# Performance work log

Measured on AMD Instinct MI355X. Metric: run time of the kernel, lower is better.

Reference implementation:

```python
import jax, jax.numpy as jnp
import numpy as np

B, S, D_MODEL, H = 4, 1024, 1024, 16
DEPTH = D_MODEL // H


def head_scales():
    # np.arange(0.1, 10 + 0.01, 9.9 / (H - 1)) -> exactly H values from 0.1 to 10.0
    return jnp.asarray(np.arange(0.1, 10 + 0.01, 9.9 / (H - 1)), dtype=jnp.float32)


def setup_inputs() -> dict:
    key = jax.random.key(0)
    ks = jax.random.split(key, 14)
    sd = 1.0 / np.sqrt(D_MODEL)
    inp = {
        "v": jax.random.normal(ks[0], (B, S, D_MODEL), jnp.float32),
        "k": jax.random.normal(ks[1], (B, S, D_MODEL), jnp.float32),
        "q": jax.random.normal(ks[2], (B, S, D_MODEL), jnp.float32),
        # pairwise distance-like weights in [0, 1)
        "weight": jax.random.uniform(ks[3], (B, S, S), jnp.float32),
        # binary padding mask, broadcastable to (B, H, S, S); 1 = masked
        "mask": (jax.random.uniform(ks[4], (B, 1, 1, S)) < 0.1).astype(jnp.float32),
        "Wq": jax.random.normal(ks[5], (D_MODEL, D_MODEL), jnp.float32) * sd,
        "bq": jnp.zeros((D_MODEL,), jnp.float32),
        "Wk": jax.random.normal(ks[6], (D_MODEL, D_MODEL), jnp.float32) * sd,
        "bk": jnp.zeros((D_MODEL,), jnp.float32),
        "Wv": jax.random.normal(ks[7], (D_MODEL, D_MODEL), jnp.float32) * sd,
        "bv": jnp.zeros((D_MODEL,), jnp.float32),
        "Wo": jax.random.normal(ks[8], (D_MODEL, D_MODEL), jnp.float32) * sd,
        "bo": jnp.zeros((D_MODEL,), jnp.float32),
    }
    return inp


def reference(v, k, q, weight, mask, Wq, bq, Wk, bk, Wv, bv, Wo, bo):
    def split_heads(x):  # (B, S, D) -> (B, H, S, depth)
        return x.reshape(B, -1, H, DEPTH).transpose(0, 2, 1, 3)

    qh = split_heads(q @ Wq + bq)
    kh = split_heads(k @ Wk + bk)
    vh = split_heads(v @ Wv + bv)

    # shift_distance[b,h,i,j] = weight[b,i,j] * scale[h]
    scales = head_scales()  # (H,)
    bias = weight[:, None, :, :] * scales[None, :, None, None]  # (B, H, S, S)

    logits = jnp.einsum("bhqd,bhkd->bhqk", qh, kh) / jnp.sqrt(
        jnp.asarray(DEPTH, jnp.float32)
    )
    logits = logits + bias + mask * (-1e9)
    attn = jax.nn.softmax(logits, axis=-1)  # (B, H, S, S)
    out = jnp.einsum("bhqk,bhkd->bhqd", attn, vh)  # (B, H, S, depth)
    out = out.transpose(0, 2, 1, 3).reshape(B, -1, D_MODEL)
    return out @ Wo + bo
```

## Files before the change

kernel.cpp:

```cpp
#include <hip/hip_runtime.h>
#include <hip/hip_fp16.h>

#define DEV __device__ __forceinline__

typedef _Float16 f16x8 __attribute__((ext_vector_type(8)));
typedef _Float16 f16x4 __attribute__((ext_vector_type(4)));
typedef float f32x4 __attribute__((ext_vector_type(4)));

DEV void gload16(void* lds, const void* g) {
  __builtin_amdgcn_global_load_lds((__attribute__((address_space(1))) const void*)g,
                                   (__attribute__((address_space(3))) void*)lds,
                                   16, 0, 0);
}

DEV f32x4 mfma16(f16x8 a, f16x8 b, f32x4 c) {
  return __builtin_amdgcn_mfma_f32_16x16x32_f16(a, b, c, 0, 0, 0);
}

DEV f16x8 cvt8(float4 a, float4 b) {
  f16x8 o;
  o[0] = (_Float16)a.x; o[1] = (_Float16)a.y; o[2] = (_Float16)a.z; o[3] = (_Float16)a.w;
  o[4] = (_Float16)b.x; o[5] = (_Float16)b.y; o[6] = (_Float16)b.z; o[7] = (_Float16)b.w;
  return o;
}

__global__ __launch_bounds__(256) void transw_kernel(
    const float* __restrict__ W0, const float* __restrict__ W1,
    const float* __restrict__ W2, const float* __restrict__ W3,
    _Float16* __restrict__ Wt) {
  __shared__ float tile[32][33];
  const float* W = (blockIdx.z == 0) ? W0 : (blockIdx.z == 1) ? W1
                 : (blockIdx.z == 2) ? W2 : W3;
  _Float16* dst = Wt + (size_t)blockIdx.z * (1024 * 1024);
  const int tx = threadIdx.x & 31, ty = threadIdx.x >> 5;
  const int n0 = blockIdx.x * 32, k0 = blockIdx.y * 32;
#pragma unroll
  for (int i = 0; i < 4; ++i)
    tile[ty + i * 8][tx] = W[(size_t)(k0 + ty + i * 8) * 1024 + n0 + tx];
  __syncthreads();
#pragma unroll
  for (int i = 0; i < 4; ++i)
    dst[(size_t)(n0 + ty + i * 8) * 1024 + k0 + tx] = (_Float16)tile[tx][ty + i * 8];
}

__global__ __launch_bounds__(256) void wcast_kernel(const float* __restrict__ W,
                                                    _Float16* __restrict__ Wh) {
  const size_t i = (size_t)(blockIdx.x * 256 + threadIdx.x) * 8;
  float4 a = *(const float4*)(W + i);
  float4 b = *(const float4*)(W + i + 4);
  *(f16x8*)(Wh + i) = cvt8(a, b);
}

__global__ __launch_bounds__(256) void qkvcast_kernel(
    const float* __restrict__ q, const float* __restrict__ k,
    const float* __restrict__ v, _Float16* __restrict__ Ah) {
  const float* src = (blockIdx.y == 0) ? q : (blockIdx.y == 1) ? k : v;
  _Float16* dst = Ah + (size_t)blockIdx.y * (4096ull * 1024);
  const size_t i = (size_t)(blockIdx.x * 256 + threadIdx.x) * 8;
  float4 a = *(const float4*)(src + i);
  float4 b = *(const float4*)(src + i + 4);
  *(f16x8*)(dst + i) = cvt8(a, b);
}

template <int BM, bool AF32>
DEV void gemm_core(const void* __restrict__ Aptr, const _Float16* __restrict__ Bt,
                   _Float16* Al, _Float16* Bl, int m0, int n0,
                   f32x4 (&acc)[4][4]) {
  constexpr int AS = AF32 ? 40 : 32;
  constexpr int WR = BM / 64, WC = 4 / WR, NI = (128 / WC) / 16;
  const int t = threadIdx.x;
  const int l = t & 63, w = t >> 6;
  const int wr = w / WC, wc = w % WC;
  const int lo = l & 15, lg = l >> 4;

  for (int ks = 0; ks < 1024; ks += 32) {
    __syncthreads();
    gload16(&Bl[t * 8], Bt + (size_t)(n0 + (t >> 2)) * 1024 + ks + (t & 3) * 8);
    gload16(&Bl[(t + 256) * 8], Bt + (size_t)(n0 + (t >> 2) + 64) * 1024 + ks + (t & 3) * 8);
    if constexpr (AF32) {
      const float* Ag = (const float*)Aptr;
      const int row = t >> 1, c0 = (t & 1) * 16;
      const float4* src = (const float4*)(Ag + (size_t)(m0 + row) * 1024 + ks + c0);
      float4 f0 = src[0], f1 = src[1], f2 = src[2], f3 = src[3];
      *(f16x8*)&Al[row * AS + c0] = cvt8(f0, f1);
      *(f16x8*)&Al[row * AS + c0 + 8] = cvt8(f2, f3);
    } else {
      const _Float16* Ag = (const _Float16*)Aptr;
      gload16(&Al[t * 8], Ag + (size_t)(m0 + (t >> 2)) * 1024 + ks + (t & 3) * 8);
      if constexpr (BM == 128)
        gload16(&Al[(t + 256) * 8], Ag + (size_t)(m0 + (t >> 2) + 64) * 1024 + ks + (t & 3) * 8);
    }
    __syncthreads();

    f16x8 af[4], bf[NI];
#pragma unroll
    for (int mi = 0; mi < 4; ++mi)
      af[mi] = *(const f16x8*)&Al[(wr * 64 + mi * 16 + lo) * AS + lg * 8];
#pragma unroll
    for (int ni = 0; ni < NI; ++ni)
      bf[ni] = *(const f16x8*)&Bl[(wc * (NI * 16) + ni * 16 + lo) * 32 + lg * 8];
#pragma unroll
    for (int mi = 0; mi < 4; ++mi)
#pragma unroll
      for (int ni = 0; ni < NI; ++ni)
        acc[mi][ni] = mfma16(af[mi], bf[ni], acc[mi][ni]);
  }
}

template <bool AHALF>
__global__ __launch_bounds__(256) void proj_kernel(
    const _Float16* __restrict__ Ah, const float* __restrict__ qin,
    const float* __restrict__ kin, const float* __restrict__ vin,
    const _Float16* __restrict__ Wt, const float* __restrict__ bq,
    const float* __restrict__ bk, const float* __restrict__ bv,
    _Float16* __restrict__ Qh, _Float16* __restrict__ Kt,
    _Float16* __restrict__ Vt) {
  __shared__ __attribute__((aligned(16))) _Float16 Al[128 * 40];
  __shared__ __attribute__((aligned(16))) _Float16 Bl[128 * 32];
  const int lin = blockIdx.x + (blockIdx.y << 3) + (blockIdx.z << 8);
  const int work = (lin & 7) * 96 + (lin >> 3);
  const int z = work >> 8;
  const int m0 = ((work & 255) >> 3) * 128;
  const int n0 = (work & 7) * 128;

  const _Float16* Bt = Wt + (size_t)z * (1 << 20);
  const float* bias = (z == 0) ? bq : (z == 1) ? bk : bv;
  _Float16* C = (z == 0) ? Qh : (z == 1) ? Kt : Vt;

  f32x4 acc[4][4];
#pragma unroll
  for (int i = 0; i < 4; ++i)
#pragma unroll
    for (int j = 0; j < 4; ++j) acc[i][j] = (f32x4){0.f, 0.f, 0.f, 0.f};
  if constexpr (AHALF) {
    gemm_core<128, false>(Ah + (size_t)z * (4096ull * 1024), Bt, Al, Bl, m0, n0, acc);
  } else {
    const float* A = (z == 0) ? qin : (z == 1) ? kin : vin;
    gemm_core<128, true>(A, Bt, Al, Bl, m0, n0, acc);
  }

  const int l = threadIdx.x & 63, w = threadIdx.x >> 6;
  const int wr = w >> 1, wc = w & 1;
  const int lo = l & 15, lg = l >> 4;
#pragma unroll
  for (int mi = 0; mi < 4; ++mi) {
#pragma unroll
    for (int ni = 0; ni < 4; ++ni) {
      const int col = n0 + wc * 64 + ni * 16 + lo;
      const int rowb = m0 + wr * 64 + mi * 16 + lg * 4;
      const float bc = bias[col];
      const int h = col >> 6, d = col & 63;
#pragma unroll
      for (int r = 0; r < 4; ++r) {
        const float vv = acc[mi][ni][r] + bc;
        const int m = rowb + r;
        const int b = m >> 10, s = m & 1023;
        const size_t slab = (size_t)(b * 16 + h) * 65536;
        if (z == 0) {
          C[slab + (size_t)s * 64 + d] = (_Float16)vv;
        } else if (z == 1) {
          C[slab + (size_t)(s >> 6) * 4096 + (size_t)(s & 63) * 64 +
            (((d >> 3) ^ (s & 7)) << 3) + (d & 7)] = (_Float16)vv;
        } else {
          C[slab + (size_t)(s >> 6) * 4096 + (size_t)d * 64 +
            ((((s >> 3) & 7) ^ (d & 7)) << 3) + (s & 7)] = (_Float16)vv;
        }
      }
    }
  }
}

__global__ __launch_bounds__(256) void outproj_kernel(
    const _Float16* __restrict__ AO, const _Float16* __restrict__ Bt,
    const float* __restrict__ bias, float* __restrict__ out) {
  __shared__ __attribute__((aligned(16))) _Float16 Al[64 * 32];
  __shared__ __attribute__((aligned(16))) _Float16 Bl[128 * 32];
  const int lin = blockIdx.x + (blockIdx.y << 3);
  const int work = (lin & 7) * 64 + (lin >> 3);
  const int m0 = (work >> 3) * 64;
  const int n0 = (work & 7) * 128;
  f32x4 acc[4][4];
#pragma unroll
  for (int i = 0; i < 4; ++i)
#pragma unroll
    for (int j = 0; j < 4; ++j) acc[i][j] = (f32x4){0.f, 0.f, 0.f, 0.f};
  gemm_core<64, false>(AO, Bt, Al, Bl, m0, n0, acc);

  const int l = threadIdx.x & 63, w = threadIdx.x >> 6;
  const int wc = w;
  const int lo = l & 15, lg = l >> 4;
#pragma unroll
  for (int mi = 0; mi < 4; ++mi) {
#pragma unroll
    for (int ni = 0; ni < 2; ++ni) {
      const int col = n0 + wc * 32 + ni * 16 + lo;
      const int rowb = m0 + mi * 16 + lg * 4;
      const float bc = bias[col];
#pragma unroll
      for (int r = 0; r < 4; ++r)
        out[(size_t)(rowb + r) * 1024 + col] = acc[mi][ni][r] + bc;
    }
  }
}

template <int NSPLIT>
__global__ __launch_bounds__(512, 4) void attn_kernel(
    const _Float16* __restrict__ Qh, const _Float16* __restrict__ Kt,
    const _Float16* __restrict__ Vt, const _Float16* __restrict__ Wh,
    const float* __restrict__ mask, void* __restrict__ Oout,
    float2* __restrict__ Sst) {
  __shared__ __attribute__((aligned(16))) _Float16 Kl[2][4096];
  __shared__ __attribute__((aligned(16))) _Float16 Vl[2][4096];
  __shared__ __attribute__((aligned(16))) _Float16 Pl[8][16][72];
  const int t = threadIdx.x, l = t & 63, w = t >> 6;
  const int lo = l & 15, lg = l >> 4;
  const int bh = blockIdx.y, b = bh >> 4, h = bh & 15;
  const int q0w = blockIdx.x * 128 + w * 16;
  const int sp = (NSPLIT > 1) ? blockIdx.z : 0;
  constexpr int NKT = 16 / NSPLIT;
  const int kt0 = sp * NKT;
  constexpr float L2E = 1.44269504089f;
  const float scale = 0.1f + (float)h * (9.9f / 15.0f);
  const float cS = 0.125f * L2E;
  const float cW = scale * L2E;
  const float cM = -1e9f * L2E;
  const _Float16* Kslab = Kt + (size_t)bh * 65536;
  const _Float16* Vslab = Vt + (size_t)bh * 65536;
  const _Float16* Wb = Wh + ((size_t)b << 20);
  const float* Mb = mask + (size_t)b * 1024;
  const int qrow = q0w + lg * 4;
  const int sl = lg ^ (lo & 7);

  const f16x8 qf0 = *(const f16x8*)(Qh + (size_t)bh * 65536 + (q0w + lo) * 64 + lg * 8);
  const f16x8 qf1 = *(const f16x8*)(Qh + (size_t)bh * 65536 + (q0w + lo) * 64 + 32 + lg * 8);

  f32x4 oacc[4];
#pragma unroll
  for (int di = 0; di < 4; ++di) oacc[di] = (f32x4){0.f, 0.f, 0.f, 0.f};
  float mrun[4], lsum[4];
#pragma unroll
  for (int r = 0; r < 4; ++r) { mrun[r] = -1e38f; lsum[r] = 0.f; }

  gload16(&Kl[0][t * 8], Kslab + (size_t)kt0 * 4096 + t * 8);
  gload16(&Vl[0][t * 8], Vslab + (size_t)kt0 * 4096 + t * 8);
  __syncthreads();

  for (int it = 0; it < NKT; ++it) {
    const int kt = kt0 + it;
    const int cur = it & 1;
    if (it + 1 < NKT) {
      gload16(&Kl[cur ^ 1][t * 8], Kslab + (size_t)(kt + 1) * 4096 + t * 8);
      gload16(&Vl[cur ^ 1][t * 8], Vslab + (size_t)(kt + 1) * 4096 + t * 8);
    }
    const int kv0 = kt * 64;
    const _Float16* Kb = Kl[cur];
    const _Float16* Vb = Vl[cur];

    float sv[4][4];
    float tm[4] = {-1e38f, -1e38f, -1e38f, -1e38f};
#pragma unroll
    for (int ni = 0; ni < 4; ++ni) {
      const int key = kv0 + ni * 16 + lo;
      const float mkv = Mb[key] * cM;
      float wgt[4];
#pragma unroll
      for (int r = 0; r < 4; ++r)
        wgt[r] = (float)Wb[(size_t)(qrow + r) * 1024 + key];
      const int kr = ni * 16 + lo;
      f16x8 kf0 = *(const f16x8*)(Kb + kr * 64 + sl * 8);
      f16x8 kf1 = *(const f16x8*)(Kb + kr * 64 + (sl ^ 4) * 8);
      f32x4 s = (f32x4){0.f, 0.f, 0.f, 0.f};
      s = mfma16(qf0, kf0, s);
      s = mfma16(qf1, kf1, s);
#pragma unroll
      for (int r = 0; r < 4; ++r) {
        const float x = s[r] * cS + wgt[r] * cW + mkv;
        sv[ni][r] = x;
        tm[r] = fmaxf(tm[r], x);
      }
    }
#pragma unroll
    for (int st = 1; st < 16; st <<= 1)
#pragma unroll
      for (int r = 0; r < 4; ++r) tm[r] = fmaxf(tm[r], __shfl_xor(tm[r], st));
    float delta = tm[0] - mrun[0];
#pragma unroll
    for (int r = 1; r < 4; ++r) delta = fmaxf(delta, tm[r] - mrun[r]);
    if (!__all(delta <= 8.0f)) {
      float fr[4];
#pragma unroll
      for (int r = 0; r < 4; ++r) {
        const float mn = fmaxf(mrun[r], tm[r]);
        fr[r] = exp2f(mrun[r] - mn);
        mrun[r] = mn;
        lsum[r] *= fr[r];
      }
#pragma unroll
      for (int di = 0; di < 4; ++di)
#pragma unroll
        for (int r = 0; r < 4; ++r) oacc[di][r] *= fr[r];
    }
#pragma unroll
    for (int ni = 0; ni < 4; ++ni)
#pragma unroll
      for (int r = 0; r < 4; ++r) {
        const float p = exp2f(sv[ni][r] - mrun[r]);
        lsum[r] += p;
        Pl[w][lg * 4 + r][ni * 16 + lo] = (_Float16)p;
      }
    const f16x8 pa0 = *(const f16x8*)(&Pl[w][lo][lg * 8]);
    const f16x8 pa1 = *(const f16x8*)(&Pl[w][lo][32 + lg * 8]);
    __builtin_amdgcn_s_setprio(1);
#pragma unroll
    for (int di = 0; di < 4; ++di) {
      const int d = di * 16 + lo;
      f16x8 vf0 = *(const f16x8*)(Vb + d * 64 + sl * 8);
      f16x8 vf1 = *(const f16x8*)(Vb + d * 64 + (sl ^ 4) * 8);
      oacc[di] = mfma16(pa0, vf0, oacc[di]);
      oacc[di] = mfma16(pa1, vf1, oacc[di]);
    }
    __builtin_amdgcn_s_setprio(0);
    __syncthreads();
  }

#pragma unroll
  for (int st = 1; st < 16; st <<= 1)
#pragma unroll
    for (int r = 0; r < 4; ++r) lsum[r] += __shfl_xor(lsum[r], st);

  if constexpr (NSPLIT > 1) {
    if (lo == 0) {
#pragma unroll
      for (int r = 0; r < 4; ++r)
        Sst[(size_t)sp * 65536 + bh * 1024 + qrow + r] = make_float2(mrun[r], lsum[r]);
    }
    _Float16* Op = (_Float16*)Oout + (size_t)sp * (64ull * 1024 * 64);
#pragma unroll
    for (int r = 0; r < 4; ++r) {
      const float inv = 1.0f / lsum[r];
#pragma unroll
      for (int di = 0; di < 4; ++di)
        Op[((size_t)bh * 1024 + qrow + r) * 64 + di * 16 + lo] =
            (_Float16)(oacc[di][r] * inv);
    }
  } else {
    _Float16* AO = (_Float16*)Oout;
#pragma unroll
    for (int r = 0; r < 4; ++r) {
      const float inv = 1.0f / lsum[r];
#pragma unroll
      for (int di = 0; di < 4; ++di)
        AO[((size_t)(b * 1024) + qrow + r) * 1024 + h * 64 + di * 16 + lo] =
            (_Float16)(oacc[di][r] * inv);
    }
  }
}

__global__ __launch_bounds__(256) void merge_kernel(
    const _Float16* __restrict__ Op, const float2* __restrict__ Sst,
    _Float16* __restrict__ AO) {
  const int idx = blockIdx.x * 256 + threadIdx.x;
  const int dc = idx & 15;
  const int qq = (idx >> 4) & 1023;
  const int bh = idx >> 14;
  const int b = bh >> 4, h = bh & 15;
  const float2 s1 = Sst[bh * 1024 + qq];
  const float2 s2 = Sst[65536 + bh * 1024 + qq];
  const float m = fmaxf(s1.x, s2.x);
  float w1 = exp2f(s1.x - m) * s1.y;
  float w2 = exp2f(s2.x - m) * s2.y;
  const float inv = 1.f / (w1 + w2);
  w1 *= inv; w2 *= inv;
  const size_t o = ((size_t)bh * 1024 + qq) * 64 + dc * 4;
  const f16x4 o1 = *(const f16x4*)(Op + o);
  const f16x4 o2 = *(const f16x4*)(Op + (64ull * 1024 * 64) + o);
  f16x4 r;
#pragma unroll
  for (int j = 0; j < 4; ++j)
    r[j] = (_Float16)(w1 * (float)o1[j] + w2 * (float)o2[j]);
  *(f16x4*)(AO + ((size_t)(b * 1024 + qq) * 1024 + h * 64 + dc * 4)) = r;
}

extern "C" void kernel_launch(void* const* d_in, const int* in_sizes, int n_in,
                              void* d_out, int out_size, void* d_ws, size_t ws_size,
                              hipStream_t stream) {
  (void)in_sizes; (void)n_in; (void)out_size;
  const float* v      = (const float*)d_in[0];
  const float* k      = (const float*)d_in[1];
  const float* q      = (const float*)d_in[2];
  const float* weight = (const float*)d_in[3];
  const float* mask   = (const float*)d_in[4];
  const float* Wq = (const float*)d_in[5];
  const float* bq = (const float*)d_in[6];
  const float* Wk = (const float*)d_in[7];
  const float* bk = (const float*)d_in[8];
  const float* Wv = (const float*)d_in[9];
  const float* bv = (const float*)d_in[10];
  const float* Wo = (const float*)d_in[11];
  const float* bo = (const float*)d_in[12];
  float* out = (float*)d_out;

  const size_t MB = 1ull << 20;
  char* ws = (char*)d_ws;
  _Float16* Wt = (_Float16*)ws;
  _Float16* Qh = (_Float16*)(ws + 8 * MB);
  _Float16* Kt = (_Float16*)(ws + 16 * MB);
  _Float16* Vt = (_Float16*)(ws + 24 * MB);
  _Float16* Wh = (_Float16*)(ws + 32 * MB);
  _Float16* Ah = (_Float16*)(ws + 40 * MB);
  _Float16* Op = (_Float16*)(ws + 40 * MB);
  float2*  Sst = (float2*)(ws + 56 * MB);
  _Float16* AO = Qh;

  transw_kernel<<<dim3(32, 32, 4), 256, 0, stream>>>(Wq, Wk, Wv, Wo, Wt);
  wcast_kernel<<<2048, 256, 0, stream>>>(weight, Wh);

  if (ws_size >= 64 * MB) {
    qkvcast_kernel<<<dim3(2048, 3), 256, 0, stream>>>(q, k, v, Ah);
    proj_kernel<true><<<dim3(8, 32, 3), 256, 0, stream>>>(Ah, q, k, v, Wt, bq, bk, bv,
                                                          Qh, Kt, Vt);
    attn_kernel<2><<<dim3(8, 64, 2), 512, 0, stream>>>(Qh, Kt, Vt, Wh, mask, Op, Sst);
    merge_kernel<<<4096, 256, 0, stream>>>(Op, Sst, AO);
    outproj_kernel<<<dim3(8, 64), 256, 0, stream>>>(AO, Wt + 3 * (1 << 20), bo, out);
  } else {
    _Float16* AO2 = (_Float16*)(ws + 40 * MB);
    proj_kernel<false><<<dim3(8, 32, 3), 256, 0, stream>>>(nullptr, q, k, v, Wt, bq, bk,
                                                           bv, Qh, Kt, Vt);
    attn_kernel<1><<<dim3(8, 64, 1), 512, 0, stream>>>(Qh, Kt, Vt, Wh, mask, AO2, nullptr);
    outproj_kernel<<<dim3(8, 64), 256, 0, stream>>>(AO2, Wt + 3 * (1 << 20), bo, out);
  }
}
```

Before: 152.6 us.

## Transpose bias weights, swizzle P scratch, and remap attention blocks to XCDs

The pairwise weight matrix is cast to fp16 transposed (key-major), so each lane fetches its four query-row bias values as one contiguous 8-byte load. Before, these were four strided scalar loads. The per-wave P staging buffer now uses an XOR-swizzled layout to cut LDS bank conflicts on the scatter-write and vector-read. In the split-K attention path, block indices are remapped so that blocks sharing the same batch-head K/V slab and split are grouped by XCD, which improves L2 reuse. The transpose-cast kernel costs more than the plain cast, and the block remap assumes the exact grid shape.

Result: slower. 157.1 us (+3.0%).

```diff
diff --git a/kernel.cpp b/kernel.cpp
--- a/kernel.cpp
+++ b/kernel.cpp
@@ -43,12 +43,20 @@
     dst[(size_t)(n0 + ty + i * 8) * 1024 + k0 + tx] = (_Float16)tile[tx][ty + i * 8];
 }
 
-__global__ __launch_bounds__(256) void wcast_kernel(const float* __restrict__ W,
-                                                    _Float16* __restrict__ Wh) {
-  const size_t i = (size_t)(blockIdx.x * 256 + threadIdx.x) * 8;
-  float4 a = *(const float4*)(W + i);
-  float4 b = *(const float4*)(W + i + 4);
-  *(f16x8*)(Wh + i) = cvt8(a, b);
+__global__ __launch_bounds__(256) void wtrans_kernel(const float* __restrict__ W,
+                                                     _Float16* __restrict__ Wht) {
+  __shared__ float tile[32][33];
+  const float* src = W + (size_t)blockIdx.z * (1024 * 1024);
+  _Float16* dst = Wht + (size_t)blockIdx.z * (1024 * 1024);
+  const int tx = threadIdx.x & 31, ty = threadIdx.x >> 5;
+  const int q0 = blockIdx.x * 32, k0 = blockIdx.y * 32;
+#pragma unroll
+  for (int i = 0; i < 4; ++i)
+    tile[ty + i * 8][tx] = src[(size_t)(q0 + ty + i * 8) * 1024 + k0 + tx];
+  __syncthreads();
+#pragma unroll
+  for (int i = 0; i < 4; ++i)
+    dst[(size_t)(k0 + ty + i * 8) * 1024 + q0 + tx] = (_Float16)tile[tx][ty + i * 8];
 }
 
 __global__ __launch_bounds__(256) void qkvcast_kernel(
@@ -206,17 +214,26 @@
 template <int NSPLIT>
 __global__ __launch_bounds__(512, 4) void attn_kernel(
     const _Float16* __restrict__ Qh, const _Float16* __restrict__ Kt,
-    const _Float16* __restrict__ Vt, const _Float16* __restrict__ Wh,
+    const _Float16* __restrict__ Vt, const _Float16* __restrict__ Wht,
     const float* __restrict__ mask, void* __restrict__ Oout,
     float2* __restrict__ Sst) {
   __shared__ __attribute__((aligned(16))) _Float16 Kl[2][4096];
   __shared__ __attribute__((aligned(16))) _Float16 Vl[2][4096];
-  __shared__ __attribute__((aligned(16))) _Float16 Pl[8][16][72];
+  __shared__ __attribute__((aligned(16))) _Float16 Pl[8][1024];
   const int t = threadIdx.x, l = t & 63, w = t >> 6;
   const int lo = l & 15, lg = l >> 4;
-  const int bh = blockIdx.y, b = bh >> 4, h = bh & 15;
-  const int q0w = blockIdx.x * 128 + w * 16;
-  const int sp = (NSPLIT > 1) ? blockIdx.z : 0;
+  int bh, qx, sp;
+  if constexpr (NSPLIT > 1) {
+    const int lin = blockIdx.x + (blockIdx.y << 3) + (blockIdx.z << 9);
+    const int xcd = lin & 7, pos = lin >> 3;
+    sp = xcd >> 2;
+    bh = (xcd & 3) * 16 + (pos & 15);
+    qx = pos >> 4;
+  } else {
+    bh = blockIdx.y; qx = blockIdx.x; sp = 0;
+  }
+  const int b = bh >> 4, h = bh & 15;
+  const int q0w = qx * 128 + w * 16;
   constexpr int NKT = 16 / NSPLIT;
   const int kt0 = sp * NKT;
   constexpr float L2E = 1.44269504089f;
@@ -226,10 +243,12 @@
   const float cM = -1e9f * L2E;
   const _Float16* Kslab = Kt + (size_t)bh * 65536;
   const _Float16* Vslab = Vt + (size_t)bh * 65536;
-  const _Float16* Wb = Wh + ((size_t)b << 20);
+  const _Float16* Wbt = Wht + ((size_t)b << 20);
   const float* Mb = mask + (size_t)b * 1024;
   const int qrow = q0w + lg * 4;
   const int sl = lg ^ (lo & 7);
+  _Float16* Plw = &Pl[w][0];
+  const int psw = lo & 7;
 
   const f16x8 qf0 = *(const f16x8*)(Qh + (size_t)bh * 65536 + (q0w + lo) * 64 + lg * 8);
   const f16x8 qf1 = *(const f16x8*)(Qh + (size_t)bh * 65536 + (q0w + lo) * 64 + 32 + lg * 8);
@@ -262,10 +281,7 @@
     for (int ni = 0; ni < 4; ++ni) {
       const int key = kv0 + ni * 16 + lo;
       const float mkv = Mb[key] * cM;
-      float wgt[4];
-#pragma unroll
-      for (int r = 0; r < 4; ++r)
-        wgt[r] = (float)Wb[(size_t)(qrow + r) * 1024 + key];
+      const f16x4 wv = *(const f16x4*)(Wbt + (size_t)key * 1024 + qrow);
       const int kr = ni * 16 + lo;
       f16x8 kf0 = *(const f16x8*)(Kb + kr * 64 + sl * 8);
       f16x8 kf1 = *(const f16x8*)(Kb + kr * 64 + (sl ^ 4) * 8);
@@ -274,7 +290,7 @@
       s = mfma16(qf1, kf1, s);
 #pragma unroll
       for (int r = 0; r < 4; ++r) {
-        const float x = s[r] * cS + wgt[r] * cW + mkv;
+        const float x = s[r] * cS + (float)wv[r] * cW + mkv;
         sv[ni][r] = x;
         tm[r] = fmaxf(tm[r], x);
       }
@@ -306,10 +322,11 @@
       for (int r = 0; r < 4; ++r) {
         const float p = exp2f(sv[ni][r] - mrun[r]);
         lsum[r] += p;
-        Pl[w][lg * 4 + r][ni * 16 + lo] = (_Float16)p;
+        const int row = lg * 4 + r;
+        Plw[row * 64 + (((ni * 2 + (lo >> 3)) ^ (row & 7)) << 3) + psw] = (_Float16)p;
       }
-    const f16x8 pa0 = *(const f16x8*)(&Pl[w][lo][lg * 8]);
-    const f16x8 pa1 = *(const f16x8*)(&Pl[w][lo][32 + lg * 8]);
+    const f16x8 pa0 = *(const f16x8*)&Plw[lo * 64 + ((lg ^ psw) << 3)];
+    const f16x8 pa1 = *(const f16x8*)&Plw[lo * 64 + (((4 + lg) ^ psw) << 3)];
     __builtin_amdgcn_s_setprio(1);
 #pragma unroll
     for (int di = 0; di < 4; ++di) {
@@ -413,7 +430,7 @@
   _Float16* AO = Qh;
 
   transw_kernel<<<dim3(32, 32, 4), 256, 0, stream>>>(Wq, Wk, Wv, Wo, Wt);
-  wcast_kernel<<<2048, 256, 0, stream>>>(weight, Wh);
+  wtrans_kernel<<<dim3(32, 32, 4), 256, 0, stream>>>(weight, Wh);
 
   if (ws_size >= 64 * MB) {
     qkvcast_kernel<<<dim3(2048, 3), 256, 0, stream>>>(q, k, v, Ah);
```
